# Kernel tuning notes

Hardware: AMD Instinct MI355X
Metric: run time of the kernel (lower is better)

Reference implementation:

```python
import jax, jax.numpy as jnp
import numpy as np
import math

N = 100000
E = 3200000
LAMDA = 0.5
ALPHA = 0.1
NLAYERS = 8


def setup_inputs() -> dict:
    key = jax.random.key(0)
    ks = jax.random.split(key, 9)
    x = jax.random.normal(ks[0], (N, 500), dtype=jnp.float32)
    row = jax.random.randint(ks[1], (E,), 0, N, dtype=jnp.int32)
    col = jax.random.randint(ks[2], (E,), 0, N, dtype=jnp.int32)
    # roughly degree-normalized positive edge weights
    edge_weight = jax.random.uniform(ks[3], (E,), dtype=jnp.float32) * (2.0 / 32.0)
    W_in = jax.random.normal(ks[4], (500, 64), dtype=jnp.float32) * (1.0 / math.sqrt(500.0))
    b_in = jnp.zeros((64,), dtype=jnp.float32)
    conv_W = jax.random.normal(ks[5], (NLAYERS, 64, 64), dtype=jnp.float32) * (1.0 / 8.0)
    W_out = jax.random.normal(ks[6], (64, 40), dtype=jnp.float32) * (1.0 / 8.0)
    b_out = jnp.zeros((40,), dtype=jnp.float32)
    return {"x": x, "row": row, "col": col, "edge_weight": edge_weight,
            "W_in": W_in, "b_in": b_in, "conv_W": conv_W,
            "W_out": W_out, "b_out": b_out}


def _spmm(row, col, w, h):
    # adj @ h with adj in COO form: gather source rows, scatter-add to dest
    msgs = h[col] * w[:, None]            # [E, nhidden]
    return jax.ops.segment_sum(msgs, row, num_segments=N)


def reference(x, row, col, edge_weight, W_in, b_in, conv_W, W_out, b_out):
    # dropout is identity in eval mode
    h0 = jax.nn.relu(x @ W_in + b_in)     # [N, nhidden]
    h = h0
    for i in range(NLAYERS):
        l = i + 1
        beta = math.log(LAMDA / l + 1.0)  # identity-mapping strength
        hi = _spmm(row, col, edge_weight, h)
        support = (1.0 - ALPHA) * hi + ALPHA * h0   # initial residual
        h = jax.nn.relu(beta * (support @ conv_W[i]) + (1.0 - beta) * support)
    logits = h @ W_out + b_out
    return jax.nn.log_softmax(logits, axis=1)
```

## Files before the change

kernel.cpp:

```cpp
#include <hip/hip_runtime.h>
#include <math.h>

#define FIN 500
#define NHID 64
#define NCLS 40
#define NLAYERS 8
#define CSHIFT 9
#define CROWS (1 << CSHIFT)
#define PTILE 16384

typedef _Float16 half4 __attribute__((ext_vector_type(4)));
typedef _Float16 half8 __attribute__((ext_vector_type(8)));


__global__ __launch_bounds__(256) void k_gemm_in(
    const float* __restrict__ x, const float* __restrict__ W,
    const float* __restrict__ b, half4* __restrict__ h0h, int n) {
  __shared__ __align__(16) float xs[32 * 68];
  __shared__ __align__(16) float ws[32 * 64];
  const int tid = threadIdx.x;
  const int row0 = blockIdx.x * 64;
  const int cj = (tid & 15) * 4;
  const int ri = (tid >> 4) * 4;
  float acc[4][4] = {};
  for (int k0 = 0; k0 < 512; k0 += 32) {
#pragma unroll
    for (int t = 0; t < 2; ++t) {
      int idx = tid + t * 256;
      int q = idx & 7;
      int r = idx >> 3;
      int gr = row0 + r; if (gr >= n) gr = n - 1;
      int gk = k0 + q * 4;
      float4 v;
      if (gk + 3 < FIN) {
        v = *reinterpret_cast<const float4*>(&x[(size_t)gr * FIN + gk]);
      } else {
        v.x = (gk + 0 < FIN) ? x[(size_t)gr * FIN + gk + 0] : 0.f;
        v.y = (gk + 1 < FIN) ? x[(size_t)gr * FIN + gk + 1] : 0.f;
        v.z = (gk + 2 < FIN) ? x[(size_t)gr * FIN + gk + 2] : 0.f;
        v.w = (gk + 3 < FIN) ? x[(size_t)gr * FIN + gk + 3] : 0.f;
      }
      int rr = r ^ (q << 2);
      xs[(q * 4 + 0) * 68 + rr] = v.x;
      xs[(q * 4 + 1) * 68 + rr] = v.y;
      xs[(q * 4 + 2) * 68 + rr] = v.z;
      xs[(q * 4 + 3) * 68 + rr] = v.w;
    }
#pragma unroll
    for (int t = 0; t < 2; ++t) {
      int idx = tid + t * 256;
      int q = idx & 15;
      int k = idx >> 4;
      int gk = k0 + k;
      float4 wv = {0.f, 0.f, 0.f, 0.f};
      if (gk < FIN) wv = *reinterpret_cast<const float4*>(&W[(size_t)gk * NHID + q * 4]);
      *reinterpret_cast<float4*>(&ws[k * 64 + q * 4]) = wv;
    }
    __syncthreads();
#pragma unroll 8
    for (int k = 0; k < 32; ++k) {
      const int s = ((k >> 2) & 7) << 2;
      const float4 wv = *reinterpret_cast<const float4*>(&ws[k * 64 + cj]);
      const float4 xv = *reinterpret_cast<const float4*>(&xs[k * 68 + (ri ^ s)]);
      const float xa[4] = {xv.x, xv.y, xv.z, xv.w};
      const float wa[4] = {wv.x, wv.y, wv.z, wv.w};
#pragma unroll
      for (int i = 0; i < 4; ++i)
#pragma unroll
        for (int j = 0; j < 4; ++j) acc[i][j] += xa[i] * wa[j];
    }
    __syncthreads();
  }
  const float4 bv = *reinterpret_cast<const float4*>(&b[cj]);
  const float ba[4] = {bv.x, bv.y, bv.z, bv.w};
#pragma unroll
  for (int i = 0; i < 4; ++i) {
    int gr = row0 + ri + i;
    if (gr < n) {
      half4 hv;
      hv.x = (_Float16)fmaxf(acc[i][0] + ba[0], 0.f);
      hv.y = (_Float16)fmaxf(acc[i][1] + ba[1], 0.f);
      hv.z = (_Float16)fmaxf(acc[i][2] + ba[2], 0.f);
      hv.w = (_Float16)fmaxf(acc[i][3] + ba[3], 0.f);
      h0h[(size_t)gr * 16 + (cj >> 2)] = hv;
    }
  }
}

__global__ __launch_bounds__(256) void k_chist(
    const int* __restrict__ row, int* __restrict__ ccnt, int e_total) {
  __shared__ int hist[256];
  const int tid = threadIdx.x;
  hist[tid] = 0;
  __syncthreads();
  const int e0 = blockIdx.x * PTILE;
  for (int t = 0; t < PTILE / 256; ++t) {
    int e = e0 + t * 256 + tid;
    if (e < e_total) atomicAdd(&hist[row[e] >> CSHIFT], 1);
  }
  __syncthreads();
  if (hist[tid]) atomicAdd(&ccnt[tid], hist[tid]);
}

__global__ __launch_bounds__(256) void k_cscan(
    const int* __restrict__ ccnt, int* __restrict__ cbase,
    int* __restrict__ bcur, int* __restrict__ ptr, int nbC, int n, int E) {
  __shared__ int sh[257];
  const int t = threadIdx.x;
  sh[t] = (t < nbC) ? ccnt[t] : 0;
  __syncthreads();
  if (t == 0) {
    int run = 0;
    for (int i = 0; i < 256; ++i) { int v = sh[i]; sh[i] = run; run += v; }
    sh[256] = run;
  }
  __syncthreads();
  if (t <= nbC) cbase[t] = sh[t];
  if (t < nbC) bcur[t] = sh[t];
  if (t == 0) ptr[n] = E;
}

__global__ __launch_bounds__(256) void k_part2(
    const int* __restrict__ row, const int* __restrict__ col,
    const float* __restrict__ w, int* __restrict__ bcurG,
    int2* __restrict__ staged, int e_total, int nbC) {
  __shared__ int hist[256];
  __shared__ int cur[256];
  const int tid = threadIdx.x;
  const int e0 = blockIdx.x * PTILE;
  if (tid < nbC) hist[tid] = 0;
  __syncthreads();
  for (int t = 0; t < PTILE / 256; ++t) {
    int e = e0 + t * 256 + tid;
    if (e < e_total) atomicAdd(&hist[row[e] >> CSHIFT], 1);
  }
  __syncthreads();
  if (tid < nbC) {
    int h = hist[tid];
    cur[tid] = h ? atomicAdd(&bcurG[tid], h) : 0;
  }
  __syncthreads();
  for (int t = 0; t < PTILE / 256; ++t) {
    int e = e0 + t * 256 + tid;
    if (e < e_total) {
      int r = row[e];
      int pos = atomicAdd(&cur[r >> CSHIFT], 1);
      staged[pos] = make_int2(((r & (CROWS - 1)) << 17) | col[e], __float_as_int(w[e]));
    }
  }
}

__global__ __launch_bounds__(256) void k_rebin3(
    const int* __restrict__ cbase, const int2* __restrict__ staged,
    int2* __restrict__ sorted, int* __restrict__ ptr, int n) {
  __shared__ int rcnt[CROWS];
  __shared__ int cur[CROWS];
  __shared__ int wsum[4];
  const int tid = threadIdx.x;
  const int r0 = blockIdx.x << CSHIFT;
  const int bstart = cbase[blockIdx.x], bend = cbase[blockIdx.x + 1];
  rcnt[tid] = 0; rcnt[tid + 256] = 0;
  __syncthreads();
  for (int i = bstart + tid; i < bend; i += 256)
    atomicAdd(&rcnt[staged[i].x >> 17], 1);
  __syncthreads();
  const int lane = tid & 63, wid = tid >> 6;
  int v0 = rcnt[2 * tid], v1 = rcnt[2 * tid + 1];
  int s = v0 + v1;
  int incl = s;
#pragma unroll
  for (int off = 1; off < 64; off <<= 1) {
    int u = __shfl_up(incl, off, 64);
    if (lane >= off) incl += u;
  }
  if (lane == 63) wsum[wid] = incl;
  __syncthreads();
  int woff = 0;
  for (int i = 0; i < wid; ++i) woff += wsum[i];
  int base = bstart + incl - s + woff;
  int rr = r0 + 2 * tid;
  if (rr < n) ptr[rr] = base;
  if (rr + 1 < n) ptr[rr + 1] = base + v0;
  cur[2 * tid] = base;
  cur[2 * tid + 1] = base + v0;
  __syncthreads();
  for (int i = bstart + tid; i < bend; i += 256) {
    int2 e = staged[i];
    int pos = atomicAdd(&cur[e.x >> 17], 1);
    sorted[pos] = make_int2(e.x & 0x1FFFF, e.y);
  }
}

__global__ __launch_bounds__(256) void k_spmm_csr(
    const int* __restrict__ ptr, const int2* __restrict__ sorted,
    const half8* __restrict__ hh, const half8* __restrict__ h0h,
    half8* __restrict__ Sh, int n) {
  const int r = blockIdx.x * 4 + (threadIdx.x >> 6);
  if (r >= n) return;
  const int lane = threadIdx.x & 63;
  const int sub = lane >> 3;
  const int fl = lane & 7;
  const int start = ptr[r], end = ptr[r + 1];
  float acc[8] = {};
  for (int e = start + sub; e < end; e += 8) {
    int2 cw = sorted[e];
    float wv = __int_as_float(cw.y);
    half8 hv = hh[(size_t)cw.x * 8 + fl];
#pragma unroll
    for (int j = 0; j < 8; ++j) acc[j] += wv * (float)hv[j];
  }
#pragma unroll
  for (int off = 8; off < 64; off <<= 1)
#pragma unroll
    for (int j = 0; j < 8; ++j) acc[j] += __shfl_xor(acc[j], off, 64);
  if (sub == 0) {
    half8 h0v = h0h[(size_t)r * 8 + fl];
    half8 o;
#pragma unroll
    for (int j = 0; j < 8; ++j)
      o[j] = (_Float16)(0.9f * acc[j] + 0.1f * (float)h0v[j]);
    Sh[(size_t)r * 8 + fl] = o;
  }
}

__global__ __launch_bounds__(256) void k_layer(
    const half8* __restrict__ Sh, const float* __restrict__ Wl,
    float* __restrict__ Af, half4* __restrict__ hout,
    float beta, int n, int write_f32) {
  __shared__ __align__(16) float st[64 * 68];
  __shared__ __align__(16) float ws[64 * 64];
  const int tid = threadIdx.x;
  const int row0 = blockIdx.x * 64;
#pragma unroll
  for (int t = 0; t < 2; ++t) {
    int idx = tid + t * 256;
    int q = idx & 7;
    int r = idx >> 3;
    int gr = row0 + r; if (gr >= n) gr = n - 1;
    half8 v = Sh[(size_t)gr * 8 + q];
#pragma unroll
    for (int jj = 0; jj < 8; ++jj) {
      int k = q * 8 + jj;
      int rr = r ^ (((k >> 2) & 7) << 2);
      st[k * 68 + rr] = (float)v[jj];
    }
  }
#pragma unroll
  for (int t = 0; t < 4; ++t) {
    int idx = tid + t * 256;
    *reinterpret_cast<float4*>(&ws[idx * 4]) = *reinterpret_cast<const float4*>(&Wl[idx * 4]);
  }
  __syncthreads();
  const int cj = (tid & 15) * 4;
  const int ri = (tid >> 4) * 4;
  float acc[4][4] = {};
#pragma unroll 8
  for (int k = 0; k < 64; ++k) {
    const int s = ((k >> 2) & 7) << 2;
    const float4 wv = *reinterpret_cast<const float4*>(&ws[k * 64 + cj]);
    const float4 sv = *reinterpret_cast<const float4*>(&st[k * 68 + (ri ^ s)]);
    const float sa[4] = {sv.x, sv.y, sv.z, sv.w};
    const float wa[4] = {wv.x, wv.y, wv.z, wv.w};
#pragma unroll
    for (int i = 0; i < 4; ++i)
#pragma unroll
      for (int j = 0; j < 4; ++j) acc[i][j] += sa[i] * wa[j];
  }
  const float g = 1.f - beta;
  const int sw = ((tid & 15) & 7) << 2;
#pragma unroll
  for (int i = 0; i < 4; ++i) {
    int gr = row0 + ri + i;
    if (gr < n) {
      float4 o;
      o.x = fmaxf(beta * acc[i][0] + g * st[(cj + 0) * 68 + ((ri + i) ^ sw)], 0.f);
      o.y = fmaxf(beta * acc[i][1] + g * st[(cj + 1) * 68 + ((ri + i) ^ sw)], 0.f);
      o.z = fmaxf(beta * acc[i][2] + g * st[(cj + 2) * 68 + ((ri + i) ^ sw)], 0.f);
      o.w = fmaxf(beta * acc[i][3] + g * st[(cj + 3) * 68 + ((ri + i) ^ sw)], 0.f);
      half4 hv; hv.x = (_Float16)o.x; hv.y = (_Float16)o.y;
      hv.z = (_Float16)o.z; hv.w = (_Float16)o.w;
      hout[(size_t)gr * 16 + (cj >> 2)] = hv;
      if (write_f32) *reinterpret_cast<float4*>(&Af[(size_t)gr * NHID + cj]) = o;
    }
  }
}

__global__ __launch_bounds__(256) void k_out(
    const float* __restrict__ h, const float* __restrict__ Wo,
    const float* __restrict__ bo, float* __restrict__ out, int n) {
  const int lane = threadIdx.x & 63;
  const int r = blockIdx.x * 4 + (threadIdx.x >> 6);
  if (r >= n) return;
  const float hv = h[(size_t)r * NHID + lane];
  const int j = (lane < NCLS) ? lane : (NCLS - 1);
  float acc = bo[j];
#pragma unroll 16
  for (int k = 0; k < NHID; ++k) {
    float hk = __shfl(hv, k, 64);
    acc += hk * Wo[k * NCLS + j];
  }
  float v = (lane < NCLS) ? acc : -INFINITY;
  float m = v;
#pragma unroll
  for (int off = 32; off; off >>= 1) m = fmaxf(m, __shfl_xor(m, off, 64));
  float e = (lane < NCLS) ? expf(acc - m) : 0.f;
  float s = e;
#pragma unroll
  for (int off = 32; off; off >>= 1) s += __shfl_xor(s, off, 64);
  if (lane < NCLS) out[(size_t)r * NCLS + lane] = acc - m - logf(s);
}

extern "C" void kernel_launch(void* const* d_in, const int* in_sizes, int n_in,
                              void* d_out, int out_size, void* d_ws, size_t ws_size,
                              hipStream_t stream) {
  const float* x  = (const float*)d_in[0];
  const int* row  = (const int*)d_in[1];
  const int* col  = (const int*)d_in[2];
  const float* ew = (const float*)d_in[3];
  const float* Wi = (const float*)d_in[4];
  const float* bi = (const float*)d_in[5];
  const float* Wc = (const float*)d_in[6];
  const float* Wo = (const float*)d_in[7];
  const float* bo = (const float*)d_in[8];
  float* out = (float*)d_out;

  const int n = in_sizes[0] / FIN;
  const int E = in_sizes[1];

  half8* h0h   = (half8*)d_ws;
  half8* hhA   = h0h + (size_t)n * 8;
  half8* hhB   = hhA + (size_t)n * 8;
  half8* Sh    = hhB + (size_t)n * 8;
  float* A     = (float*)(Sh + (size_t)n * 8);
  int2*  staged= (int2*)A;
  int2*  sorted= (int2*)(A + (size_t)n * NHID);
  int*   ptr   = (int*)(sorted + E);
  int*   ccnt  = ptr + (n + 1);
  int*   cbase = ccnt + 256;
  int*   bcur  = cbase + 257;

  const int nbC = (n + CROWS - 1) >> CSHIFT;
  const int nPB = (E + PTILE - 1) / PTILE;
  dim3 blk(256);

  hipMemsetAsync(ccnt, 0, 256 * sizeof(int), stream);
  k_chist<<<dim3(nPB), blk, 0, stream>>>(row, ccnt, E);
  k_cscan<<<dim3(1), blk, 0, stream>>>(ccnt, cbase, bcur, ptr, nbC, n, E);
  k_part2<<<dim3(nPB), blk, 0, stream>>>(row, col, ew, bcur, staged, E, nbC);
  k_rebin3<<<dim3(nbC), blk, 0, stream>>>(cbase, staged, sorted, ptr, n);

  k_gemm_in<<<dim3((n + 63) / 64), blk, 0, stream>>>(x, Wi, bi, (half4*)h0h, n);

  const half8* hin = h0h;
  for (int l = 0; l < NLAYERS; ++l) {
    half8* hout = (l & 1) ? hhB : hhA;
    k_spmm_csr<<<dim3((n + 3) / 4), blk, 0, stream>>>(ptr, sorted, hin, h0h, Sh, n);
    float beta = logf(0.5f / (float)(l + 1) + 1.f);
    k_layer<<<dim3((n + 63) / 64), blk, 0, stream>>>(
        Sh, Wc + (size_t)l * NHID * NHID, A, (half4*)hout, beta, n,
        (l == NLAYERS - 1) ? 1 : 0);
    hin = hout;
  }
  k_out<<<dim3((n + 3) / 4), blk, 0, stream>>>(A, Wo, bo, out, n);
}
```

Before: 1.269 ms.

## Use MFMA fp16 matrix cores for input and layer GEMMs, unroll SpMM gathers

Replaces the LDS-tiled fp32 FMA GEMMs in the input projection and per-layer transforms with __builtin_amdgcn_mfma_f32_16x16x32_f16. A new prep kernel transposes and converts the weights to fp16. Input x is converted to fp16 on the fly. The SpMM inner loop is unrolled by four so more gathers are in flight, and the h0 load is hoisted. The final layer now writes fp16 only and k_out reads that, which adds fp16 rounding to the input GEMM and the last hidden state.

Result: faster. 1.232 ms (-2.9%).

```diff
diff --git a/kernel.cpp b/kernel.cpp
--- a/kernel.cpp
+++ b/kernel.cpp
@@ -9,80 +9,69 @@
 #define CROWS (1 << CSHIFT)
 #define PTILE 16384
 
-typedef _Float16 half4 __attribute__((ext_vector_type(4)));
 typedef _Float16 half8 __attribute__((ext_vector_type(8)));
-
+typedef float f32x4 __attribute__((ext_vector_type(4)));
+
+__global__ __launch_bounds__(256) void k_prep(
+    const float* __restrict__ Wi, const float* __restrict__ Wc,
+    _Float16* __restrict__ WtIn, _Float16* __restrict__ WcT) {
+  const int t = blockIdx.x * 256 + threadIdx.x;
+  const int stride = gridDim.x * 256;
+  for (int i = t; i < 64 * 512; i += stride) {
+    int c = i >> 9, k = i & 511;
+    WtIn[i] = (k < FIN) ? (_Float16)Wi[k * 64 + c] : (_Float16)0.f;
+  }
+  for (int i = t; i < NLAYERS * 64 * 64; i += stride) {
+    int l = i >> 12, rem = i & 4095, c = rem >> 6, k = rem & 63;
+    WcT[i] = (_Float16)Wc[l * 4096 + k * 64 + c];
+  }
+}
 
 __global__ __launch_bounds__(256) void k_gemm_in(
-    const float* __restrict__ x, const float* __restrict__ W,
-    const float* __restrict__ b, half4* __restrict__ h0h, int n) {
-  __shared__ __align__(16) float xs[32 * 68];
-  __shared__ __align__(16) float ws[32 * 64];
-  const int tid = threadIdx.x;
-  const int row0 = blockIdx.x * 64;
-  const int cj = (tid & 15) * 4;
-  const int ri = (tid >> 4) * 4;
-  float acc[4][4] = {};
+    const float* __restrict__ x, const _Float16* __restrict__ Wt,
+    const float* __restrict__ b, _Float16* __restrict__ h0, int n) {
+  const int lane = threadIdx.x & 63;
+  const int wv = threadIdx.x >> 6;
+  const int row0 = blockIdx.x * 64 + wv * 16;
+  const int arow = row0 + (lane & 15);
+  const int gr = (arow < n) ? arow : (n - 1);
+  const int kg = (lane >> 4) * 8;
+  const float* xrow = x + (size_t)gr * FIN;
+  f32x4 acc[4];
+#pragma unroll
+  for (int ct = 0; ct < 4; ++ct) acc[ct] = (f32x4){0.f, 0.f, 0.f, 0.f};
   for (int k0 = 0; k0 < 512; k0 += 32) {
-#pragma unroll
-    for (int t = 0; t < 2; ++t) {
-      int idx = tid + t * 256;
-      int q = idx & 7;
-      int r = idx >> 3;
-      int gr = row0 + r; if (gr >= n) gr = n - 1;
-      int gk = k0 + q * 4;
-      float4 v;
-      if (gk + 3 < FIN) {
-        v = *reinterpret_cast<const float4*>(&x[(size_t)gr * FIN + gk]);
-      } else {
-        v.x = (gk + 0 < FIN) ? x[(size_t)gr * FIN + gk + 0] : 0.f;
-        v.y = (gk + 1 < FIN) ? x[(size_t)gr * FIN + gk + 1] : 0.f;
-        v.z = (gk + 2 < FIN) ? x[(size_t)gr * FIN + gk + 2] : 0.f;
-        v.w = (gk + 3 < FIN) ? x[(size_t)gr * FIN + gk + 3] : 0.f;
-      }
-      int rr = r ^ (q << 2);
-      xs[(q * 4 + 0) * 68 + rr] = v.x;
-      xs[(q * 4 + 1) * 68 + rr] = v.y;
-      xs[(q * 4 + 2) * 68 + rr] = v.z;
-      xs[(q * 4 + 3) * 68 + rr] = v.w;
-    }
-#pragma unroll
-    for (int t = 0; t < 2; ++t) {
-      int idx = tid + t * 256;
-      int q = idx & 15;
-      int k = idx >> 4;
-      int gk = k0 + k;
-      float4 wv = {0.f, 0.f, 0.f, 0.f};
-      if (gk < FIN) wv = *reinterpret_cast<const float4*>(&W[(size_t)gk * NHID + q * 4]);
-      *reinterpret_cast<float4*>(&ws[k * 64 + q * 4]) = wv;
-    }
-    __syncthreads();
-#pragma unroll 8
-    for (int k = 0; k < 32; ++k) {
-      const int s = ((k >> 2) & 7) << 2;
-      const float4 wv = *reinterpret_cast<const float4*>(&ws[k * 64 + cj]);
-      const float4 xv = *reinterpret_cast<const float4*>(&xs[k * 68 + (ri ^ s)]);
-      const float xa[4] = {xv.x, xv.y, xv.z, xv.w};
-      const float wa[4] = {wv.x, wv.y, wv.z, wv.w};
-#pragma unroll
-      for (int i = 0; i < 4; ++i)
-#pragma unroll
-        for (int j = 0; j < 4; ++j) acc[i][j] += xa[i] * wa[j];
-    }
-    __syncthreads();
-  }
-  const float4 bv = *reinterpret_cast<const float4*>(&b[cj]);
-  const float ba[4] = {bv.x, bv.y, bv.z, bv.w};
-#pragma unroll
-  for (int i = 0; i < 4; ++i) {
-    int gr = row0 + ri + i;
-    if (gr < n) {
-      half4 hv;
-      hv.x = (_Float16)fmaxf(acc[i][0] + ba[0], 0.f);
-      hv.y = (_Float16)fmaxf(acc[i][1] + ba[1], 0.f);
-      hv.z = (_Float16)fmaxf(acc[i][2] + ba[2], 0.f);
-      hv.w = (_Float16)fmaxf(acc[i][3] + ba[3], 0.f);
-      h0h[(size_t)gr * 16 + (cj >> 2)] = hv;
+    const int gk = k0 + kg;
+    half8 a;
+    if (gk + 7 < FIN) {
+      float4 u = *reinterpret_cast<const float4*>(xrow + gk);
+      float4 v = *reinterpret_cast<const float4*>(xrow + gk + 4);
+      a[0] = (_Float16)u.x; a[1] = (_Float16)u.y;
+      a[2] = (_Float16)u.z; a[3] = (_Float16)u.w;
+      a[4] = (_Float16)v.x; a[5] = (_Float16)v.y;
+      a[6] = (_Float16)v.z; a[7] = (_Float16)v.w;
+    } else {
+#pragma unroll
+      for (int j = 0; j < 8; ++j)
+        a[j] = (gk + j < FIN) ? (_Float16)xrow[gk + j] : (_Float16)0.f;
+    }
+#pragma unroll
+    for (int ct = 0; ct < 4; ++ct) {
+      const half8 bf = *reinterpret_cast<const half8*>(
+          Wt + (size_t)(ct * 16 + (lane & 15)) * 512 + gk);
+      acc[ct] = __builtin_amdgcn_mfma_f32_16x16x32_f16(a, bf, acc[ct], 0, 0, 0);
+    }
+  }
+  const int orow = row0 + (lane >> 4) * 4;
+#pragma unroll
+  for (int ct = 0; ct < 4; ++ct) {
+    const int c = ct * 16 + (lane & 15);
+    const float bb = b[c];
+#pragma unroll
+    for (int i = 0; i < 4; ++i) {
+      const int rr = orow + i;
+      if (rr < n)
+        h0[(size_t)rr * NHID + c] = (_Float16)fmaxf(acc[ct][i] + bb, 0.f);
     }
   }
 }
@@ -201,11 +190,31 @@
   const int sub = lane >> 3;
   const int fl = lane & 7;
   const int start = ptr[r], end = ptr[r + 1];
+  const half8 h0v = h0h[(size_t)r * 8 + fl];
   float acc[8] = {};
-  for (int e = start + sub; e < end; e += 8) {
-    int2 cw = sorted[e];
-    float wv = __int_as_float(cw.y);
-    half8 hv = hh[(size_t)cw.x * 8 + fl];
+  int e = start + sub;
+  for (; e + 24 < end; e += 32) {
+    const int2 c0 = sorted[e];
+    const int2 c1 = sorted[e + 8];
+    const int2 c2 = sorted[e + 16];
+    const int2 c3 = sorted[e + 24];
+    const half8 v0 = hh[(size_t)c0.x * 8 + fl];
+    const half8 v1 = hh[(size_t)c1.x * 8 + fl];
+    const half8 v2 = hh[(size_t)c2.x * 8 + fl];
+    const half8 v3 = hh[(size_t)c3.x * 8 + fl];
+    const float w0 = __int_as_float(c0.y);
+    const float w1 = __int_as_float(c1.y);
+    const float w2 = __int_as_float(c2.y);
+    const float w3 = __int_as_float(c3.y);
+#pragma unroll
+    for (int j = 0; j < 8; ++j)
+      acc[j] += w0 * (float)v0[j] + w1 * (float)v1[j] +
+                w2 * (float)v2[j] + w3 * (float)v3[j];
+  }
+  for (; e < end; e += 8) {
+    const int2 cw = sorted[e];
+    const float wv = __int_as_float(cw.y);
+    const half8 hv = hh[(size_t)cw.x * 8 + fl];
 #pragma unroll
     for (int j = 0; j < 8; ++j) acc[j] += wv * (float)hv[j];
   }
@@ -214,7 +223,6 @@
 #pragma unroll
     for (int j = 0; j < 8; ++j) acc[j] += __shfl_xor(acc[j], off, 64);
   if (sub == 0) {
-    half8 h0v = h0h[(size_t)r * 8 + fl];
     half8 o;
 #pragma unroll
     for (int j = 0; j < 8; ++j)
@@ -224,74 +232,51 @@
 }
 
 __global__ __launch_bounds__(256) void k_layer(
-    const half8* __restrict__ Sh, const float* __restrict__ Wl,
-    float* __restrict__ Af, half4* __restrict__ hout,
-    float beta, int n, int write_f32) {
-  __shared__ __align__(16) float st[64 * 68];
-  __shared__ __align__(16) float ws[64 * 64];
-  const int tid = threadIdx.x;
-  const int row0 = blockIdx.x * 64;
-#pragma unroll
-  for (int t = 0; t < 2; ++t) {
-    int idx = tid + t * 256;
-    int q = idx & 7;
-    int r = idx >> 3;
-    int gr = row0 + r; if (gr >= n) gr = n - 1;
-    half8 v = Sh[(size_t)gr * 8 + q];
-#pragma unroll
-    for (int jj = 0; jj < 8; ++jj) {
-      int k = q * 8 + jj;
-      int rr = r ^ (((k >> 2) & 7) << 2);
-      st[k * 68 + rr] = (float)v[jj];
-    }
-  }
-#pragma unroll
-  for (int t = 0; t < 4; ++t) {
-    int idx = tid + t * 256;
-    *reinterpret_cast<float4*>(&ws[idx * 4]) = *reinterpret_cast<const float4*>(&Wl[idx * 4]);
-  }
-  __syncthreads();
-  const int cj = (tid & 15) * 4;
-  const int ri = (tid >> 4) * 4;
-  float acc[4][4] = {};
-#pragma unroll 8
-  for (int k = 0; k < 64; ++k) {
-    const int s = ((k >> 2) & 7) << 2;
-    const float4 wv = *reinterpret_cast<const float4*>(&ws[k * 64 + cj]);
-    const float4 sv = *reinterpret_cast<const float4*>(&st[k * 68 + (ri ^ s)]);
-    const float sa[4] = {sv.x, sv.y, sv.z, sv.w};
-    const float wa[4] = {wv.x, wv.y, wv.z, wv.w};
-#pragma unroll
-    for (int i = 0; i < 4; ++i)
-#pragma unroll
-      for (int j = 0; j < 4; ++j) acc[i][j] += sa[i] * wa[j];
+    const _Float16* __restrict__ Sh, const _Float16* __restrict__ Wt,
+    _Float16* __restrict__ hout, float beta, int n) {
+  const int lane = threadIdx.x & 63;
+  const int wv = threadIdx.x >> 6;
+  const int row0 = blockIdx.x * 64 + wv * 16;
+  const int arow = row0 + (lane & 15);
+  const int gr = (arow < n) ? arow : (n - 1);
+  const int kg = (lane >> 4) * 8;
+  const half8 a0 = *reinterpret_cast<const half8*>(Sh + (size_t)gr * NHID + kg);
+  const half8 a1 = *reinterpret_cast<const half8*>(Sh + (size_t)gr * NHID + 32 + kg);
+  f32x4 acc[4];
+#pragma unroll
+  for (int ct = 0; ct < 4; ++ct) acc[ct] = (f32x4){0.f, 0.f, 0.f, 0.f};
+#pragma unroll
+  for (int ct = 0; ct < 4; ++ct) {
+    const int c = ct * 16 + (lane & 15);
+    const half8 b0 = *reinterpret_cast<const half8*>(Wt + c * NHID + kg);
+    const half8 b1 = *reinterpret_cast<const half8*>(Wt + c * NHID + 32 + kg);
+    acc[ct] = __builtin_amdgcn_mfma_f32_16x16x32_f16(a0, b0, acc[ct], 0, 0, 0);
+    acc[ct] = __builtin_amdgcn_mfma_f32_16x16x32_f16(a1, b1, acc[ct], 0, 0, 0);
   }
   const float g = 1.f - beta;
-  const int sw = ((tid & 15) & 7) << 2;
-#pragma unroll
-  for (int i = 0; i < 4; ++i) {
-    int gr = row0 + ri + i;
-    if (gr < n) {
-      float4 o;
-      o.x = fmaxf(beta * acc[i][0] + g * st[(cj + 0) * 68 + ((ri + i) ^ sw)], 0.f);
-      o.y = fmaxf(beta * acc[i][1] + g * st[(cj + 1) * 68 + ((ri + i) ^ sw)], 0.f);
-      o.z = fmaxf(beta * acc[i][2] + g * st[(cj + 2) * 68 + ((ri + i) ^ sw)], 0.f);
-      o.w = fmaxf(beta * acc[i][3] + g * st[(cj + 3) * 68 + ((ri + i) ^ sw)], 0.f);
-      half4 hv; hv.x = (_Float16)o.x; hv.y = (_Float16)o.y;
-      hv.z = (_Float16)o.z; hv.w = (_Float16)o.w;
-      hout[(size_t)gr * 16 + (cj >> 2)] = hv;
-      if (write_f32) *reinterpret_cast<float4*>(&Af[(size_t)gr * NHID + cj]) = o;
+  const int orow = row0 + (lane >> 4) * 4;
+#pragma unroll
+  for (int ct = 0; ct < 4; ++ct) {
+    const int c = ct * 16 + (lane & 15);
+#pragma unroll
+    for (int i = 0; i < 4; ++i) {
+      const int rr = orow + i;
+      if (rr < n) {
+        const float s = (float)Sh[(size_t)rr * NHID + c];
+        hout[(size_t)rr * NHID + c] =
+            (_Float16)fmaxf(beta * acc[ct][i] + g * s, 0.f);
+      }
     }
   }
 }
 
 __global__ __launch_bounds__(256) void k_out(
-    const float* __restrict__ h, const float* __restrict__ Wo,
+    const _Float16* __restrict__ h, const float* __restrict__ Wo,
     const float* __restrict__ bo, float* __restrict__ out, int n) {
   const int lane = threadIdx.x & 63;
   const int r = blockIdx.x * 4 + (threadIdx.x >> 6);
   if (r >= n) return;
-  const float hv = h[(size_t)r * NHID + lane];
+  const float hv = (float)h[(size_t)r * NHID + lane];
   const int j = (lane < NCLS) ? lane : (NCLS - 1);
   float acc = bo[j];
 #pragma unroll 16
@@ -333,6 +318,8 @@
   half8* Sh    = hhB + (size_t)n * 8;
   float* A     = (float*)(Sh + (size_t)n * 8);
   int2*  staged= (int2*)A;
+  _Float16* WtIn = (_Float16*)A;
+  _Float16* WcT  = WtIn + 64 * 512;
   int2*  sorted= (int2*)(A + (size_t)n * NHID);
   int*   ptr   = (int*)(sorted + E);
   int*   ccnt  = ptr + (n + 1);
@@ -349,7 +336,9 @@
   k_part2<<<dim3(nPB), blk, 0, stream>>>(row, col, ew, bcur, staged, E, nbC);
   k_rebin3<<<dim3(nbC), blk, 0, stream>>>(cbase, staged, sorted, ptr, n);
 
-  k_gemm_in<<<dim3((n + 63) / 64), blk, 0, stream>>>(x, Wi, bi, (half4*)h0h, n);
+  k_prep<<<dim3(64), blk, 0, stream>>>(Wi, Wc, WtIn, WcT);
+
+  k_gemm_in<<<dim3((n + 63) / 64), blk, 0, stream>>>(x, WtIn, bi, (_Float16*)h0h, n);
 
   const half8* hin = h0h;
   for (int l = 0; l < NLAYERS; ++l) {
@@ -357,9 +346,8 @@
     k_spmm_csr<<<dim3((n + 3) / 4), blk, 0, stream>>>(ptr, sorted, hin, h0h, Sh, n);
     float beta = logf(0.5f / (float)(l + 1) + 1.f);
     k_layer<<<dim3((n + 63) / 64), blk, 0, stream>>>(
-        Sh, Wc + (size_t)l * NHID * NHID, A, (half4*)hout, beta, n,
-        (l == NLAYERS - 1) ? 1 : 0);
+        (const _Float16*)Sh, WcT + (size_t)l * NHID * NHID, (_Float16*)hout, beta, n);
     hin = hout;
   }
-  k_out<<<dim3((n + 3) / 4), blk, 0, stream>>>(A, Wo, bo, out, n);
-}
+  k_out<<<dim3((n + 3) / 4), blk, 0, stream>>>((const _Float16*)hin, Wo, bo, out, n);
+}
```
